# Performance work log

Hardware: AMD Instinct MI355X
Metric: run time of the kernel (lower is better)

The kernel has to match this reference:

```python
import jax, jax.numpy as jnp
import numpy as np

EMBED_DIM = 2048
NUM_HEADS = 32
HEAD_DIM = EMBED_DIM // NUM_HEADS
SCALE = HEAD_DIM ** -0.5
B, S = 2, 2048


def setup_inputs() -> dict:
    key = jax.random.key(0)
    ks = jax.random.split(key, 9)
    std = EMBED_DIM ** -0.5
    inp = {
        "h": jax.random.normal(ks[0], (B, S, EMBED_DIM), dtype=jnp.float32),
        "Wq": jax.random.normal(ks[1], (EMBED_DIM, EMBED_DIM), dtype=jnp.float32) * std,
        "bq": jax.random.normal(ks[2], (EMBED_DIM,), dtype=jnp.float32) * 0.02,
        "Wk": jax.random.normal(ks[3], (EMBED_DIM, EMBED_DIM), dtype=jnp.float32) * std,
        "bk": jax.random.normal(ks[4], (EMBED_DIM,), dtype=jnp.float32) * 0.02,
        "Wv": jax.random.normal(ks[5], (EMBED_DIM, EMBED_DIM), dtype=jnp.float32) * std,
        "bv": jax.random.normal(ks[6], (EMBED_DIM,), dtype=jnp.float32) * 0.02,
        "Wo": jax.random.normal(ks[7], (EMBED_DIM, EMBED_DIM), dtype=jnp.float32) * std,
        "bo": jax.random.normal(ks[8], (EMBED_DIM,), dtype=jnp.float32) * 0.02,
    }
    return inp


def reference(h, Wq, bq, Wk, bk, Wv, bv, Wo, bo):
    # QKV projections (nn.Linear: x @ W.T + b)
    q = h @ Wq.T + bq  # [B, S, E]
    k = h @ Wk.T + bk
    v = h @ Wv.T + bv
    # split heads
    q = q.reshape(B, S, NUM_HEADS, HEAD_DIM)
    k = k.reshape(B, S, NUM_HEADS, HEAD_DIM)
    v = v.reshape(B, S, NUM_HEADS, HEAD_DIM)
    # scaled dot-product attention with causal (tril) mask
    scores = jnp.einsum("bqhd,bkhd->bhqk", q, k) * SCALE  # [B, H, S, S]
    causal = jnp.tril(jnp.ones((S, S), dtype=bool))  # [S, S]
    neg = jnp.finfo(scores.dtype).min
    scores = jnp.where(causal[None, None, :, :], scores, neg)
    attn = jax.nn.softmax(scores, axis=-1)
    o = jnp.einsum("bhqk,bkhd->bqhd", attn, v).reshape(B, S, EMBED_DIM)
    return o @ Wo.T + bo
```

## Files before the change

kernel.cpp:

```cpp
#include <hip/hip_runtime.h>
#include <hip/hip_bf16.h>
#include <stdint.h>

#define EMBED 2048
#define NHEADS 32
#define HDIM 64
#define BATCH 2
#define SEQ 2048
#define ATT_SCALE 0.125f
#define LOG2E 1.4426950408889634f

typedef __attribute__((ext_vector_type(8))) short bf16x8;
typedef __attribute__((ext_vector_type(4))) float f32x4;
typedef __attribute__((ext_vector_type(16))) float f32x16;
typedef __attribute__((ext_vector_type(4))) unsigned short u16x4;
typedef __attribute__((ext_vector_type(2))) unsigned int u32x2;

static __device__ __forceinline__ unsigned short f2bf(float f) {
  union { float f; uint32_t u; } v; v.f = f;
  uint32_t r = v.u + 0x7fffu + ((v.u >> 16) & 1u);
  return (unsigned short)(r >> 16);
}

static __device__ __forceinline__ void gload_lds16(const unsigned short* g, unsigned short* l) {
  __builtin_amdgcn_global_load_lds(
      (const __attribute__((address_space(1))) unsigned int*)g,
      (__attribute__((address_space(3))) unsigned int*)l, 16, 0, 0);
}

__global__ void cvt_all(const float* __restrict__ h,
                        const float* __restrict__ Wq, const float* __restrict__ Wk,
                        const float* __restrict__ Wv, const float* __restrict__ Wo,
                        unsigned short* __restrict__ out) {
  const int n4 = 6291456;
  int idx = blockIdx.x * blockDim.x + threadIdx.x;
  int stride = gridDim.x * blockDim.x;
  for (int i = idx; i < n4; i += stride) {
    const float* src; int off;
    if (i < 2097152)      { src = h;  off = i; }
    else if (i < 3145728) { src = Wq; off = i - 2097152; }
    else if (i < 4194304) { src = Wk; off = i - 3145728; }
    else if (i < 5242880) { src = Wv; off = i - 4194304; }
    else                  { src = Wo; off = i - 5242880; }
    float4 v = ((const float4*)src)[off];
    u16x4 o;
    o.x = f2bf(v.x); o.y = f2bf(v.y); o.z = f2bf(v.z); o.w = f2bf(v.w);
    ((u16x4*)out)[i] = o;
  }
}

template<int MODE, int NBJ>
__global__ __launch_bounds__(512, 2)
void gemm8(const unsigned short* __restrict__ A,
           const unsigned short* __restrict__ W,
           const float* __restrict__ b0, const float* __restrict__ b1,
           const float* __restrict__ b2,
           unsigned short* __restrict__ o0, unsigned short* __restrict__ o1,
           unsigned short* __restrict__ o2,
           float* __restrict__ fo, float qscale) {
  __shared__ unsigned short lds[2][24576];
  const int tid = threadIdx.x;
  const int w = tid >> 6, l = tid & 63;
  const int wm = w >> 1, wn = w & 1;
  const int r16 = l & 15, g = l >> 4;
  const int nblk = 16 * NBJ;
  const int swz = (blockIdx.x & 7) * (nblk >> 3) + (blockIdx.x >> 3);
  const int bi = swz / NBJ, bj = swz % NBJ;
  const int arow0 = bi * 256, bcol0 = bj * 128;

  f32x4 acc[4][4];
#pragma unroll
  for (int i = 0; i < 4; ++i)
#pragma unroll
    for (int j = 0; j < 4; ++j) acc[i][j] = (f32x4){0.f, 0.f, 0.f, 0.f};

  const int lrow = l >> 3;
  const int gcu = ((l & 7) ^ lrow) * 8;

  auto stageA = [&](int buf, int t, int mq, int call) {
    const int m = call * 8 + w;
    const int row0 = mq * 32 + (m >> 2) * 64 + (m & 3) * 8;
    gload_lds16(A + (size_t)(arow0 + row0 + lrow) * 2048 + t * 64 + gcu,
                &lds[buf][row0 * 64]);
  };
  auto stageB = [&](int buf, int t, int nq) {
    const int row0 = nq * 32 + (w >> 2) * 64 + (w & 3) * 8;
    gload_lds16(W + (size_t)(bcol0 + row0 + lrow) * 2048 + t * 64 + gcu,
                &lds[buf][16384 + row0 * 64]);
  };
  auto ldA = [&](int buf, int mf, int ks) -> bf16x8 {
    const int row = wm * 64 + mf * 16 + r16;
    const int u = (ks * 4 + g) ^ (r16 & 7);
    return *(const bf16x8*)&lds[buf][row * 64 + u * 8];
  };
  auto ldB = [&](int buf, int nf, int ks) -> bf16x8 {
    const int row = wn * 64 + nf * 16 + r16;
    const int u = (ks * 4 + g) ^ (r16 & 7);
    return *(const bf16x8*)&lds[buf][16384 + row * 64 + u * 8];
  };

  stageA(0, 0, 0, 0); stageA(0, 0, 0, 1); stageB(0, 0, 0);
  stageA(0, 0, 1, 0); stageA(0, 0, 1, 1); stageB(0, 0, 1);
  stageA(1, 1, 0, 0); stageA(1, 1, 0, 1); stageB(1, 1, 0);
  asm volatile("s_waitcnt vmcnt(3)" ::: "memory");
  __builtin_amdgcn_sched_barrier(0);
  __builtin_amdgcn_s_barrier();

  bf16x8 af[2][2], bf[4][2];

#define MMA_Q(MQ, NQ)                                                          \
  __builtin_amdgcn_s_setprio(1);                                               \
  _Pragma("unroll")                                                            \
  for (int i = 0; i < 2; ++i)                                                  \
    _Pragma("unroll")                                                          \
    for (int j = 0; j < 2; ++j)                                                \
      _Pragma("unroll")                                                        \
      for (int ks = 0; ks < 2; ++ks)                                           \
        acc[(MQ)*2 + i][(NQ)*2 + j] = __builtin_amdgcn_mfma_f32_16x16x32_bf16( \
            af[i][ks], bf[(NQ)*2 + j][ks], acc[(MQ)*2 + i][(NQ)*2 + j], 0, 0, 0); \
  __builtin_amdgcn_s_setprio(0);

  const int nt = 32;
  for (int c = 0; c < nt; ++c) {
    const int X = c & 1;
    const bool s1 = (c + 1 < nt), s2 = (c + 2 < nt);
    af[0][0] = ldA(X, 0, 0); af[0][1] = ldA(X, 0, 1);
    af[1][0] = ldA(X, 1, 0); af[1][1] = ldA(X, 1, 1);
    bf[0][0] = ldB(X, 0, 0); bf[0][1] = ldB(X, 0, 1);
    bf[1][0] = ldB(X, 1, 0); bf[1][1] = ldB(X, 1, 1);
    if (s1) { stageA(X ^ 1, c + 1, 1, 0); stageA(X ^ 1, c + 1, 1, 1); }
    MMA_Q(0, 0);
    __builtin_amdgcn_s_barrier();
    bf[2][0] = ldB(X, 2, 0); bf[2][1] = ldB(X, 2, 1);
    bf[3][0] = ldB(X, 3, 0); bf[3][1] = ldB(X, 3, 1);
    if (s1) stageB(X ^ 1, c + 1, 1);
    MMA_Q(0, 1);
    __builtin_amdgcn_s_barrier();
    af[0][0] = ldA(X, 2, 0); af[0][1] = ldA(X, 2, 1);
    af[1][0] = ldA(X, 3, 0); af[1][1] = ldA(X, 3, 1);
    if (s2) { stageA(X, c + 2, 0, 0); stageA(X, c + 2, 0, 1); }
    MMA_Q(1, 0);
    __builtin_amdgcn_s_barrier();
    if (s2) stageB(X, c + 2, 0);
    MMA_Q(1, 1);
    if (s2) asm volatile("s_waitcnt vmcnt(3)" ::: "memory");
    else    asm volatile("s_waitcnt vmcnt(0)" ::: "memory");
    __builtin_amdgcn_sched_barrier(0);
    __builtin_amdgcn_s_barrier();
  }
#undef MMA_Q

#pragma unroll
  for (int mf = 0; mf < 4; ++mf) {
    const int irow = arow0 + wm * 64 + mf * 16 + g * 4;
#pragma unroll
    for (int nf = 0; nf < 4; ++nf) {
      const int jcol = bcol0 + wn * 64 + nf * 16 + r16;
      if (MODE == 1) {
        const float bval = b0[jcol];
#pragma unroll
        for (int rr = 0; rr < 4; ++rr)
          fo[(size_t)(irow + rr) * 2048 + jcol] = acc[mf][nf][rr] + bval;
      } else {
        const int which = bj >> 4;
        const int jl = jcol & 2047;
        const int hh = jl >> 6, d = jl & 63;
        const float bval = (which == 0) ? b0[jl] : (which == 1) ? b1[jl] : b2[jl];
        const float osc = (which == 0) ? qscale : 1.0f;
        unsigned short* outp = (which == 0) ? o0 : (which == 1) ? o1 : o2;
#pragma unroll
        for (int rr = 0; rr < 4; ++rr) {
          const float val = (acc[mf][nf][rr] + bval) * osc;
          const int i = irow + rr;
          const int b = i >> 11, s = i & 2047;
          size_t off;
          if (which < 2) off = (((size_t)(b * NHEADS + hh)) * SEQ + s) * HDIM + d;
          else           off = (((size_t)(b * NHEADS + hh)) * HDIM + d) * SEQ + s;
          outp[off] = f2bf(val);
        }
      }
    }
  }
}

__global__ __launch_bounds__(256, 2)
void attn_kernel(const unsigned short* __restrict__ Q,
                 const unsigned short* __restrict__ K,
                 const unsigned short* __restrict__ Vt,
                 unsigned short* __restrict__ O) {
  __shared__ unsigned short K_lds[2][64 * 72];
  __shared__ unsigned short V_lds[2][64 * 72];
  __shared__ __align__(16) float abuf[4][32];
  __shared__ __align__(16) float lbuf[4][32];
  const int tid = threadIdx.x;
  const int w = tid >> 6, l = tid & 63;
  const int q5 = l & 31, hi = l >> 5;
  const int bid = ((blockIdx.x & 7) << 6) | (blockIdx.x >> 3);
  const int pair = bid & 7;
  const int bh = bid >> 3;
  const unsigned short* Qh = Q + (size_t)bh * SEQ * HDIM;
  const unsigned short* Kh = K + (size_t)bh * SEQ * HDIM;
  const unsigned short* Vh = Vt + (size_t)bh * HDIM * SEQ;
  const int bq = bh >> 5, hh = bh & 31;
  const int srow = tid >> 3;
  const int scol = (tid & 7) * 8;

  for (int half = 0; half < 2; ++half) {
    const int qt = half ? (15 - pair) : pair;
    const int wrow0 = qt * 128 + w * 32;
    const int wrow_max = wrow0 + 31;
    const int n_tiles = 2 * qt + 2;
    const int qrow = wrow0 + q5;

    bf16x8 qf[4];
#pragma unroll
    for (int ks = 0; ks < 4; ++ks)
      qf[ks] = *(const bf16x8*)(Qh + (size_t)qrow * HDIM + ks * 16 + hi * 8);

    f32x16 oacc[2];
#pragma unroll
    for (int df = 0; df < 2; ++df)
#pragma unroll
      for (int r = 0; r < 16; ++r) oacc[df][r] = 0.f;
    float m_run = -3.0e38f, l_run = 0.f;

    bf16x8 kreg[2], vreg[2];
#pragma unroll
    for (int j = 0; j < 2; ++j) {
      const int rr = j * 32 + srow;
      kreg[j] = *(const bf16x8*)(Kh + (size_t)rr * HDIM + scol);
      vreg[j] = *(const bf16x8*)(Vh + (size_t)rr * SEQ + scol);
    }
    __syncthreads();
#pragma unroll
    for (int j = 0; j < 2; ++j) {
      const int rr = j * 32 + srow;
      *(bf16x8*)(K_lds[0] + rr * 72 + scol) = kreg[j];
      *(bf16x8*)(V_lds[0] + rr * 72 + scol) = vreg[j];
    }

    for (int t = 0; t < n_tiles; ++t) {
      const int cur = t & 1;
      const bool not_last = (t + 1 < n_tiles);
      if (not_last) {
#pragma unroll
        for (int j = 0; j < 2; ++j) {
          const int rr = j * 32 + srow;
          kreg[j] = *(const bf16x8*)(Kh + (size_t)((t + 1) * 64 + rr) * HDIM + scol);
          vreg[j] = *(const bf16x8*)(Vh + (size_t)rr * SEQ + (t + 1) * 64 + scol);
        }
      }
      __syncthreads();

      if (t * 64 <= wrow_max) {
        f32x16 skf[2];
#pragma unroll
        for (int kf = 0; kf < 2; ++kf)
#pragma unroll
          for (int r = 0; r < 16; ++r) skf[kf][r] = 0.f;
        __builtin_amdgcn_s_setprio(1);
#pragma unroll
        for (int kf = 0; kf < 2; ++kf)
#pragma unroll
          for (int ks = 0; ks < 4; ++ks) {
            bf16x8 ak = *(const bf16x8*)(K_lds[cur] + (kf * 32 + q5) * 72 + ks * 16 + hi * 8);
            skf[kf] = __builtin_amdgcn_mfma_f32_32x32x16_bf16(ak, qf[ks], skf[kf], 0, 0, 0);
          }
        __builtin_amdgcn_s_setprio(0);

        const bool need_mask = (t * 64 + 63 > wrow0);
        if (need_mask) {
#pragma unroll
          for (int kf = 0; kf < 2; ++kf)
#pragma unroll
            for (int r = 0; r < 16; ++r) {
              const int key = t * 64 + kf * 32 + (r & 3) + 8 * (r >> 2) + 4 * hi;
              if (key > qrow) skf[kf][r] = -3.0e38f;
            }
        }

        float mx = -3.0e38f;
#pragma unroll
        for (int kf = 0; kf < 2; ++kf)
#pragma unroll
          for (int r = 0; r < 16; ++r) mx = fmaxf(mx, skf[kf][r]);
        mx = fmaxf(mx, __shfl_xor(mx, 32));

        if (__any(mx > m_run + 8.0f)) {
          const float mnew = fmaxf(m_run, mx);
          const float alpha = exp2f(m_run - mnew);
          m_run = mnew;
          l_run *= alpha;
          if (l < 32) abuf[w][l] = alpha;
          f32x4 av[4];
#pragma unroll
          for (int k = 0; k < 4; ++k)
            av[k] = *(const f32x4*)&abuf[w][8 * k + 4 * hi];
#pragma unroll
          for (int df = 0; df < 2; ++df)
#pragma unroll
            for (int r = 0; r < 16; ++r) oacc[df][r] *= av[r >> 2][r & 3];
        }

        unsigned int pkA[8], pkB[8];
        float psum = 0.f;
#pragma unroll
        for (int kf = 0; kf < 2; ++kf)
#pragma unroll
          for (int rr = 0; rr < 4; ++rr) {
            unsigned int pb[4];
#pragma unroll
            for (int j = 0; j < 4; ++j) {
              const float p = exp2f(skf[kf][rr * 4 + j] - m_run);
              psum += p;
              union { float f; unsigned int u; } c; c.f = p;
              pb[j] = c.u + 0x8000u;
            }
            pkA[kf * 4 + rr] = __builtin_amdgcn_perm(pb[1], pb[0], 0x07060302);
            pkB[kf * 4 + rr] = __builtin_amdgcn_perm(pb[3], pb[2], 0x07060302);
          }
        psum += __shfl_xor(psum, 32);
        l_run += psum;

        __builtin_amdgcn_s_setprio(1);
#pragma unroll
        for (int ks = 0; ks < 4; ++ks) {
          u32x2 ra = __builtin_amdgcn_permlane32_swap(pkA[2 * ks], pkA[2 * ks + 1], false, false);
          u32x2 rb = __builtin_amdgcn_permlane32_swap(pkB[2 * ks], pkB[2 * ks + 1], false, false);
          union { unsigned int u[4]; bf16x8 v; } pa;
          pa.u[0] = ra.x; pa.u[1] = rb.x; pa.u[2] = ra.y; pa.u[3] = rb.y;
#pragma unroll
          for (int df = 0; df < 2; ++df) {
            bf16x8 vf = *(const bf16x8*)(V_lds[cur] + (df * 32 + q5) * 72 + ks * 16 + hi * 8);
            oacc[df] = __builtin_amdgcn_mfma_f32_32x32x16_bf16(pa.v, vf, oacc[df], 0, 0, 0);
          }
        }
        __builtin_amdgcn_s_setprio(0);
      }

      if (not_last) {
#pragma unroll
        for (int j = 0; j < 2; ++j) {
          const int rr = j * 32 + srow;
          *(bf16x8*)(K_lds[cur ^ 1] + rr * 72 + scol) = kreg[j];
          *(bf16x8*)(V_lds[cur ^ 1] + rr * 72 + scol) = vreg[j];
        }
      }
    }

    if (l < 32) lbuf[w][l] = l_run;
    f32x4 lv[4];
#pragma unroll
    for (int k = 0; k < 4; ++k)
      lv[k] = *(const f32x4*)&lbuf[w][8 * k + 4 * hi];
#pragma unroll
    for (int df = 0; df < 2; ++df) {
      const int d = df * 32 + q5;
#pragma unroll
      for (int r = 0; r < 16; ++r) {
        const int s = wrow0 + (r & 3) + 8 * (r >> 2) + 4 * hi;
        const float inv = __builtin_amdgcn_rcpf(lv[r >> 2][r & 3]);
        O[((size_t)(bq * SEQ + s)) * EMBED + hh * HDIM + d] = f2bf(oacc[df][r] * inv);
      }
    }
  }
}

extern "C" void kernel_launch(void* const* d_in, const int* in_sizes, int n_in,
                              void* d_out, int out_size, void* d_ws, size_t ws_size,
                              hipStream_t stream) {
  const float* h  = (const float*)d_in[0];
  const float* Wq = (const float*)d_in[1];
  const float* bq = (const float*)d_in[2];
  const float* Wk = (const float*)d_in[3];
  const float* bk = (const float*)d_in[4];
  const float* Wv = (const float*)d_in[5];
  const float* bv = (const float*)d_in[6];
  const float* Wo = (const float*)d_in[7];
  const float* bo = (const float*)d_in[8];

  if (ws_size < (size_t)117440512) return;

  unsigned short* ws = (unsigned short*)d_ws;
  unsigned short* hb = ws;
  unsigned short* wqb = ws + 8388608;
  unsigned short* wob = ws + 20971520;
  unsigned short* Qw  = ws + 25165824;
  unsigned short* Kw  = ws + 33554432;
  unsigned short* Vw  = ws + 41943040;
  unsigned short* Ow  = ws + 50331648;

  cvt_all<<<2048, 256, 0, stream>>>(h, Wq, Wk, Wv, Wo, ws);

  const float qscale = ATT_SCALE * LOG2E;
  gemm8<0, 48><<<768, 512, 0, stream>>>(hb, wqb, bq, bk, bv, Qw, Kw, Vw, nullptr, qscale);

  attn_kernel<<<512, 256, 0, stream>>>(Qw, Kw, Vw, Ow);

  gemm8<1, 16><<<256, 512, 0, stream>>>(Ow, wob, bo, bo, bo, nullptr, nullptr, nullptr,
                                        (float*)d_out, 1.0f);
}
```

Measured before the change: 246.0 us.

## Use 256x256 tiles with XCD-aware block mapping for the QKV GEMM

```diff
diff --git a/kernel.cpp b/kernel.cpp
--- a/kernel.cpp
+++ b/kernel.cpp
@@ -49,21 +49,145 @@
   }
 }
 
-template<int MODE, int NBJ>
 __global__ __launch_bounds__(512, 2)
-void gemm8(const unsigned short* __restrict__ A,
-           const unsigned short* __restrict__ W,
-           const float* __restrict__ b0, const float* __restrict__ b1,
-           const float* __restrict__ b2,
-           unsigned short* __restrict__ o0, unsigned short* __restrict__ o1,
-           unsigned short* __restrict__ o2,
-           float* __restrict__ fo, float qscale) {
+void gemm256_qkv(const unsigned short* __restrict__ A,
+                 const unsigned short* __restrict__ W,
+                 const float* __restrict__ b0, const float* __restrict__ b1,
+                 const float* __restrict__ b2,
+                 unsigned short* __restrict__ o0, unsigned short* __restrict__ o1,
+                 unsigned short* __restrict__ o2, float qscale) {
+  __shared__ unsigned short lds[2][32768];
+  const int tid = threadIdx.x;
+  const int w = tid >> 6, l = tid & 63;
+  const int wm = w >> 2, wn = w & 3;
+  const int r16 = l & 15, g = l >> 4;
+  const int xcd = blockIdx.x & 7, t8 = blockIdx.x >> 3;
+  const int bi = (xcd >> 2) * 8 + (t8 & 7);
+  const int bj = (xcd & 3) * 6 + (t8 >> 3);
+  const int arow0 = bi * 256, bcol0 = bj * 256;
+
+  f32x4 acc[8][4];
+#pragma unroll
+  for (int i = 0; i < 8; ++i)
+#pragma unroll
+    for (int j = 0; j < 4; ++j) acc[i][j] = (f32x4){0.f, 0.f, 0.f, 0.f};
+
+  const int lr8 = (l >> 3) & 7;
+  const int gcu = ((l & 7) ^ lr8) * 8;
+  const int wb = (w & 3) * 8 + (w >> 2) * 64;
+
+  auto stageA = [&](int buf, int kt, int base) {
+    gload_lds16(A + (size_t)(arow0 + base + (tid >> 3)) * 2048 + kt * 64 + gcu,
+                &lds[buf][(base + w * 8) * 64]);
+  };
+  auto stageB = [&](int buf, int kt, int nh, int k) {
+    const int rbase = wb + nh * 32 + k * 128;
+    gload_lds16(W + (size_t)(bcol0 + rbase + (l >> 3)) * 2048 + kt * 64 + gcu,
+                &lds[buf][16384 + rbase * 64]);
+  };
+  auto ldA = [&](int buf, int mf, int ks) -> bf16x8 {
+    const int row = wm * 128 + mf * 16 + r16;
+    const int u = (ks * 4 + g) ^ (r16 & 7);
+    return *(const bf16x8*)&lds[buf][row * 64 + u * 8];
+  };
+  auto ldB = [&](int buf, int nf, int ks) -> bf16x8 {
+    const int row = wn * 64 + nf * 16 + r16;
+    const int u = (ks * 4 + g) ^ (r16 & 7);
+    return *(const bf16x8*)&lds[buf][16384 + row * 64 + u * 8];
+  };
+
+  bf16x8 af[4][2], bfr[4][2];
+
+#define MMA_Q(MH, NH)                                                              \
+  __builtin_amdgcn_s_setprio(1);                                                   \
+  _Pragma("unroll")                                                                \
+  for (int i = 0; i < 4; ++i)                                                      \
+    _Pragma("unroll")                                                              \
+    for (int j = 0; j < 2; ++j)                                                    \
+      _Pragma("unroll")                                                            \
+      for (int ks = 0; ks < 2; ++ks)                                               \
+        acc[(MH)*4 + i][(NH)*2 + j] = __builtin_amdgcn_mfma_f32_16x16x32_bf16(     \
+            af[i][ks], bfr[(NH)*2 + j][ks], acc[(MH)*4 + i][(NH)*2 + j], 0, 0, 0); \
+  __builtin_amdgcn_s_setprio(0);
+
+  stageB(0, 0, 0, 0); stageB(0, 0, 0, 1);
+  stageB(0, 0, 1, 0); stageB(0, 0, 1, 1);
+  stageA(0, 0, 0); stageA(0, 0, 128);
+  stageA(0, 0, 64); stageA(0, 0, 192);
+  asm volatile("s_waitcnt vmcnt(2)" ::: "memory");
+  __builtin_amdgcn_sched_barrier(0);
+  __builtin_amdgcn_s_barrier();
+
+  const int nt = 32;
+  for (int c = 0; c < nt; ++c) {
+    const int X = c & 1, Y = X ^ 1;
+    const bool s1 = (c + 1 < nt);
+#pragma unroll
+    for (int i = 0; i < 4; ++i) { af[i][0] = ldA(X, i, 0); af[i][1] = ldA(X, i, 1); }
+#pragma unroll
+    for (int j = 0; j < 2; ++j) { bfr[j][0] = ldB(X, j, 0); bfr[j][1] = ldB(X, j, 1); }
+    if (s1) { stageB(Y, c + 1, 0, 0); stageB(Y, c + 1, 0, 1); }
+    MMA_Q(0, 0);
+    __builtin_amdgcn_s_barrier();
+#pragma unroll
+    for (int j = 2; j < 4; ++j) { bfr[j][0] = ldB(X, j, 0); bfr[j][1] = ldB(X, j, 1); }
+    if (s1) { stageB(Y, c + 1, 1, 0); stageB(Y, c + 1, 1, 1); }
+    MMA_Q(0, 1);
+    __builtin_amdgcn_s_barrier();
+    if (s1) asm volatile("s_waitcnt vmcnt(4)" ::: "memory");
+    else    asm volatile("s_waitcnt vmcnt(0)" ::: "memory");
+    __builtin_amdgcn_sched_barrier(0);
+#pragma unroll
+    for (int i = 0; i < 4; ++i) { af[i][0] = ldA(X, i + 4, 0); af[i][1] = ldA(X, i + 4, 1); }
+    if (s1) { stageA(Y, c + 1, 0); stageA(Y, c + 1, 128); }
+    MMA_Q(1, 0);
+    __builtin_amdgcn_s_barrier();
+    if (s1) { stageA(Y, c + 1, 64); stageA(Y, c + 1, 192); }
+    MMA_Q(1, 1);
+    if (s1) asm volatile("s_waitcnt vmcnt(2)" ::: "memory");
+    else    asm volatile("s_waitcnt vmcnt(0)" ::: "memory");
+    __builtin_amdgcn_sched_barrier(0);
+    __builtin_amdgcn_s_barrier();
+  }
+#undef MMA_Q
+
+  const int which = bj >> 3;
+  const float* bb = (which == 0) ? b0 : (which == 1) ? b1 : b2;
+  const float osc = (which == 0) ? qscale : 1.0f;
+  unsigned short* outp = (which == 0) ? o0 : (which == 1) ? o1 : o2;
+#pragma unroll
+  for (int mf = 0; mf < 8; ++mf) {
+    const int irow = arow0 + wm * 128 + mf * 16 + g * 4;
+#pragma unroll
+    for (int nf = 0; nf < 4; ++nf) {
+      const int jcol = bcol0 + wn * 64 + nf * 16 + r16;
+      const int jl = jcol & 2047;
+      const int hh = jl >> 6, d = jl & 63;
+      const float bval = bb[jl];
+#pragma unroll
+      for (int rr = 0; rr < 4; ++rr) {
+        const float val = (acc[mf][nf][rr] + bval) * osc;
+        const int i = irow + rr;
+        const int b = i >> 11, s = i & 2047;
+        size_t off;
+        if (which < 2) off = (((size_t)(b * NHEADS + hh)) * SEQ + s) * HDIM + d;
+        else           off = (((size_t)(b * NHEADS + hh)) * HDIM + d) * SEQ + s;
+        outp[off] = f2bf(val);
+      }
+    }
+  }
+}
+
+__global__ __launch_bounds__(512, 2)
+void gemm8_out(const unsigned short* __restrict__ A,
+               const unsigned short* __restrict__ W,
+               const float* __restrict__ bias, float* __restrict__ fo) {
   __shared__ unsigned short lds[2][24576];
   const int tid = threadIdx.x;
   const int w = tid >> 6, l = tid & 63;
   const int wm = w >> 1, wn = w & 1;
   const int r16 = l & 15, g = l >> 4;
-  const int nblk = 16 * NBJ;
+  const int NBJ = 16, nblk = 256;
   const int swz = (blockIdx.x & 7) * (nblk >> 3) + (blockIdx.x >> 3);
   const int bi = swz / NBJ, bj = swz % NBJ;
   const int arow0 = bi * 256, bcol0 = bj * 128;
@@ -106,7 +230,7 @@
   __builtin_amdgcn_sched_barrier(0);
   __builtin_amdgcn_s_barrier();
 
-  bf16x8 af[2][2], bf[4][2];
+  bf16x8 af[2][2], bfr[4][2];
 
 #define MMA_Q(MQ, NQ)                                                          \
   __builtin_amdgcn_s_setprio(1);                                               \
@@ -117,7 +241,7 @@
       _Pragma("unroll")                                                        \
       for (int ks = 0; ks < 2; ++ks)                                           \
         acc[(MQ)*2 + i][(NQ)*2 + j] = __builtin_amdgcn_mfma_f32_16x16x32_bf16( \
-            af[i][ks], bf[(NQ)*2 + j][ks], acc[(MQ)*2 + i][(NQ)*2 + j], 0, 0, 0); \
+            af[i][ks], bfr[(NQ)*2 + j][ks], acc[(MQ)*2 + i][(NQ)*2 + j], 0, 0, 0); \
   __builtin_amdgcn_s_setprio(0);
 
   const int nt = 32;
@@ -126,13 +250,13 @@
     const bool s1 = (c + 1 < nt), s2 = (c + 2 < nt);
     af[0][0] = ldA(X, 0, 0); af[0][1] = ldA(X, 0, 1);
     af[1][0] = ldA(X, 1, 0); af[1][1] = ldA(X, 1, 1);
-    bf[0][0] = ldB(X, 0, 0); bf[0][1] = ldB(X, 0, 1);
-    bf[1][0] = ldB(X, 1, 0); bf[1][1] = ldB(X, 1, 1);
+    bfr[0][0] = ldB(X, 0, 0); bfr[0][1] = ldB(X, 0, 1);
+    bfr[1][0] = ldB(X, 1, 0); bfr[1][1] = ldB(X, 1, 1);
     if (s1) { stageA(X ^ 1, c + 1, 1, 0); stageA(X ^ 1, c + 1, 1, 1); }
     MMA_Q(0, 0);
     __builtin_amdgcn_s_barrier();
-    bf[2][0] = ldB(X, 2, 0); bf[2][1] = ldB(X, 2, 1);
-    bf[3][0] = ldB(X, 3, 0); bf[3][1] = ldB(X, 3, 1);
+    bfr[2][0] = ldB(X, 2, 0); bfr[2][1] = ldB(X, 2, 1);
+    bfr[3][0] = ldB(X, 3, 0); bfr[3][1] = ldB(X, 3, 1);
     if (s1) stageB(X ^ 1, c + 1, 1);
     MMA_Q(0, 1);
     __builtin_amdgcn_s_barrier();
@@ -156,29 +280,10 @@
 #pragma unroll
     for (int nf = 0; nf < 4; ++nf) {
       const int jcol = bcol0 + wn * 64 + nf * 16 + r16;
-      if (MODE == 1) {
-        const float bval = b0[jcol];
-#pragma unroll
-        for (int rr = 0; rr < 4; ++rr)
-          fo[(size_t)(irow + rr) * 2048 + jcol] = acc[mf][nf][rr] + bval;
-      } else {
-        const int which = bj >> 4;
-        const int jl = jcol & 2047;
-        const int hh = jl >> 6, d = jl & 63;
-        const float bval = (which == 0) ? b0[jl] : (which == 1) ? b1[jl] : b2[jl];
-        const float osc = (which == 0) ? qscale : 1.0f;
-        unsigned short* outp = (which == 0) ? o0 : (which == 1) ? o1 : o2;
-#pragma unroll
-        for (int rr = 0; rr < 4; ++rr) {
-          const float val = (acc[mf][nf][rr] + bval) * osc;
-          const int i = irow + rr;
-          const int b = i >> 11, s = i & 2047;
-          size_t off;
-          if (which < 2) off = (((size_t)(b * NHEADS + hh)) * SEQ + s) * HDIM + d;
-          else           off = (((size_t)(b * NHEADS + hh)) * HDIM + d) * SEQ + s;
-          outp[off] = f2bf(val);
-        }
-      }
+      const float bval = bias[jcol];
+#pragma unroll
+      for (int rr = 0; rr < 4; ++rr)
+        fo[(size_t)(irow + rr) * 2048 + jcol] = acc[mf][nf][rr] + bval;
     }
   }
 }
@@ -393,10 +498,9 @@
   cvt_all<<<2048, 256, 0, stream>>>(h, Wq, Wk, Wv, Wo, ws);
 
   const float qscale = ATT_SCALE * LOG2E;
-  gemm8<0, 48><<<768, 512, 0, stream>>>(hb, wqb, bq, bk, bv, Qw, Kw, Vw, nullptr, qscale);
+  gemm256_qkv<<<384, 512, 0, stream>>>(hb, wqb, bq, bk, bv, Qw, Kw, Vw, qscale);
 
   attn_kernel<<<512, 256, 0, stream>>>(Qw, Kw, Vw, Ow);
 
-  gemm8<1, 16><<<256, 512, 0, stream>>>(Ow, wob, bo, bo, bo, nullptr, nullptr, nullptr,
-                                        (float*)d_out, 1.0f);
-}
+  gemm8_out<<<256, 512, 0, stream>>>(Ow, wob, bo, (float*)d_out);
+}
```

New measurement: 276.1 us. 1.12x slower.
